# Performance work log

Measured on AMD Instinct MI355X. Metric: run time of the kernel, lower is better.

## Reference

```python
import jax, jax.numpy as jnp
import numpy as np

N_HEADS = 16
D_HEAD = 64
D_MODEL = 1024
WINDOW = 256
B, T = 4, 2048


def rotate_half(x):
    x1, x2 = jnp.split(x, 2, axis=-1)
    return jnp.concatenate([-x2, x1], axis=-1)


def apply_rope(x, cos, sin):
    return x * cos + rotate_half(x) * sin


def setup_inputs() -> dict:
    key = jax.random.key(0)
    ks = jax.random.split(key, 5)
    x = jax.random.normal(ks[0], (B, T, D_MODEL), dtype=jnp.float32)
    cos = jax.random.normal(ks[1], (1, T, 1, D_HEAD), dtype=jnp.float32)
    sin = jax.random.normal(ks[2], (1, T, 1, D_HEAD), dtype=jnp.float32)
    qkv_w = jax.random.normal(ks[3], (3 * D_MODEL, D_MODEL), dtype=jnp.float32) * (D_MODEL ** -0.5)
    out_w = jax.random.normal(ks[4], (D_MODEL, D_MODEL), dtype=jnp.float32) * (D_MODEL ** -0.5)
    return {"x": x, "cos": cos, "sin": sin, "qkv_w": qkv_w, "out_w": out_w}


def reference(x, cos, sin, qkv_w, out_w):
    Bc, Tc, C = x.shape
    # QKV projection (bias-free Linear: y = x @ W^T)
    qkv = jnp.einsum('btc,fc->btf', x, qkv_w)
    q, k, v = jnp.split(qkv, 3, axis=-1)
    # [B, H, T, d]
    def to_heads(t):
        return t.reshape(Bc, Tc, N_HEADS, D_HEAD).transpose(0, 2, 1, 3)
    q, k, v = to_heads(q), to_heads(k), to_heads(v)
    # RoPE: cos/sin [1, T, 1, d] -> [1, 1, T, d] broadcasting over heads
    cos_t = cos[:, :Tc].transpose(0, 2, 1, 3)
    sin_t = sin[:, :Tc].transpose(0, 2, 1, 3)
    q = apply_rope(q, cos_t, sin_t)
    k = apply_rope(k, cos_t, sin_t)
    # banded causal mask: allow j <= i and j >= i - (window-1)
    i = jnp.arange(Tc)[:, None]
    j = jnp.arange(Tc)[None, :]
    allowed = (j <= i) & (j >= i - (WINDOW - 1))  # [T, T]
    scale = 1.0 / jnp.sqrt(jnp.asarray(D_HEAD, dtype=q.dtype))
    scores = jnp.einsum('bhqd,bhkd->bhqk', q, k) * scale
    scores = jnp.where(allowed[None, None], scores, jnp.finfo(scores.dtype).min)
    attn = jax.nn.softmax(scores, axis=-1)
    out = jnp.einsum('bhqk,bhkd->bhqd', attn, v)
    out = out.transpose(0, 2, 1, 3).reshape(Bc, Tc, C)
    return jnp.einsum('btc,oc->bto', out, out_w)
```

## Files before the change

### kernel.cpp

```cpp
#include <hip/hip_runtime.h>

typedef __bf16 bf16_t;
typedef __bf16 bf16x8 __attribute__((ext_vector_type(8)));
typedef __bf16 bf16x4 __attribute__((ext_vector_type(4)));
typedef float f32x4 __attribute__((ext_vector_type(4)));

#define GLOAD_LDS16(gptr, lptr)                                                              \
  __builtin_amdgcn_global_load_lds((const __attribute__((address_space(1))) void*)(gptr),    \
                                   (__attribute__((address_space(3))) void*)(lptr), 16, 0, 0)

__device__ __forceinline__ f32x4 f32x4_zero() {
  f32x4 v; v[0] = 0.f; v[1] = 0.f; v[2] = 0.f; v[3] = 0.f; return v;
}

__device__ __forceinline__ int kxr(int r) { return (r & 7) ^ (((r >> 3) & 3) << 1); }

__global__ void cast3_kernel(const float* __restrict__ a, const float* __restrict__ b,
                             const float* __restrict__ c, bf16_t* __restrict__ oa,
                             bf16_t* __restrict__ ob, bf16_t* __restrict__ oc) {
  int i = blockIdx.x * blockDim.x + threadIdx.x;
  const float* src; bf16_t* dst; int j;
  if (i < 2097152) { src = a; dst = oa; j = i; }
  else if (i < 2883584) { src = b; dst = ob; j = i - 2097152; }
  else { src = c; dst = oc; j = i - 2883584; }
  float4 v = ((const float4*)src)[j];
  bf16x4 o;
  o[0] = (bf16_t)v.x; o[1] = (bf16_t)v.y; o[2] = (bf16_t)v.z; o[3] = (bf16_t)v.w;
  ((bf16x4*)dst)[j] = o;
}

template <int MODE>
__global__ __launch_bounds__(256) void gemm_bt_kernel(
    const bf16_t* __restrict__ A, const bf16_t* __restrict__ B, float* __restrict__ C,
    bf16_t* __restrict__ oq, bf16_t* __restrict__ ok_, bf16_t* __restrict__ ov,
    const float* __restrict__ cosp, const float* __restrict__ sinp,
    int M, int N, int K) {
  constexpr int BM = 128, BN = 128, BK = 32;
  __shared__ bf16_t As[BM * BK];
  __shared__ bf16_t Bs[BN * BK];
  const int tid = threadIdx.x;
  const int lane = tid & 63;
  const int wid = tid >> 6;
  const int wm = (wid >> 1) * 64;
  const int wn = (wid & 1) * 64;
  const int l16 = lane & 15;
  const int qd = lane >> 4;
  const int bm = blockIdx.x, bn = blockIdx.y;

  const int srow = tid >> 2;
  const int skol = (tid & 3) * 8;

  const bf16_t* gA = A + (size_t)(bm * BM + srow) * K + skol;
  const bf16_t* gB = B + (size_t)(bn * BN + srow) * K + skol;
  bf16_t* lA = &As[srow * BK + skol];
  bf16_t* lB = &Bs[srow * BK + skol];

  f32x4 acc[4][4];
#pragma unroll
  for (int mb = 0; mb < 4; mb++)
#pragma unroll
    for (int nb = 0; nb < 4; nb++) acc[mb][nb] = f32x4_zero();

  for (int k0 = 0; k0 < K; k0 += BK) {
    __syncthreads();
    GLOAD_LDS16(gA + k0, lA);
    GLOAD_LDS16(gA + (size_t)64 * K + k0, lA + 64 * BK);
    GLOAD_LDS16(gB + k0, lB);
    GLOAD_LDS16(gB + (size_t)64 * K + k0, lB + 64 * BK);
    __syncthreads();

    bf16x8 af[4], bfr[4];
#pragma unroll
    for (int mb = 0; mb < 4; mb++)
      af[mb] = *(const bf16x8*)&As[(wm + mb * 16 + l16) * BK + qd * 8];
#pragma unroll
    for (int nb = 0; nb < 4; nb++)
      bfr[nb] = *(const bf16x8*)&Bs[(wn + nb * 16 + l16) * BK + qd * 8];
#pragma unroll
    for (int mb = 0; mb < 4; mb++)
#pragma unroll
      for (int nb = 0; nb < 4; nb++)
        acc[mb][nb] = __builtin_amdgcn_mfma_f32_16x16x32_bf16(af[mb], bfr[nb], acc[mb][nb], 0, 0, 0);
  }

  if (MODE == 0) {
#pragma unroll
    for (int mb = 0; mb < 4; mb++)
#pragma unroll
      for (int nb = 0; nb < 4; nb++)
#pragma unroll
        for (int r = 0; r < 4; r++) {
          int row = bm * BM + wm + mb * 16 + qd * 4 + r;
          int col = bn * BN + wn + nb * 16 + l16;
          C[(size_t)row * N + col] = acc[mb][nb][r];
        }
  } else {
    const int part = bn >> 3;
    const int h = ((bn * 128 + wn) & 1023) >> 6;
    bf16_t* dst = (part == 0) ? oq : (part == 1) ? ok_ : ov;
    if (part == 2) {
#pragma unroll
      for (int mb = 0; mb < 4; mb++)
#pragma unroll
        for (int r = 0; r < 4; r++) {
          int row = bm * BM + wm + mb * 16 + qd * 4 + r;
          int b = row >> 11, t = row & 2047;
          size_t basei = (((size_t)(b * 16 + h)) * 2048 + t) * 64;
#pragma unroll
          for (int nb = 0; nb < 4; nb++)
            dst[basei + nb * 16 + l16] = (bf16_t)acc[mb][nb][r];
        }
    } else {
      const float qsc = (part == 0) ? 0.18033688011112042f : 1.0f;
#pragma unroll
      for (int mb = 0; mb < 4; mb++)
#pragma unroll
        for (int r = 0; r < 4; r++) {
          int row = bm * BM + wm + mb * 16 + qd * 4 + r;
          int b = row >> 11, t = row & 2047;
          size_t basei = (((size_t)(b * 16 + h)) * 2048 + t) * 64;
#pragma unroll
          for (int nb = 0; nb < 2; nb++) {
            int d = nb * 16 + l16;
            float xl = acc[mb][nb][r];
            float xh = acc[mb][nb + 2][r];
            float cl = cosp[t * 64 + d], ch = cosp[t * 64 + d + 32];
            float sl = sinp[t * 64 + d], sh = sinp[t * 64 + d + 32];
            dst[basei + d]      = (bf16_t)((xl * cl - xh * sl) * qsc);
            dst[basei + d + 32] = (bf16_t)((xh * ch + xl * sh) * qsc);
          }
        }
    }
  }
}

__global__ __launch_bounds__(256) void attn_kernel(
    const bf16_t* __restrict__ qh, const bf16_t* __restrict__ kh,
    const bf16_t* __restrict__ vh, bf16_t* __restrict__ ao) {
  __shared__ bf16_t qs[64 * 64];
  __shared__ bf16_t ks[64 * 64];
  __shared__ bf16_t vs[64 * 64];
  __shared__ bf16_t vswz[8 * 64 * 8];
  __shared__ bf16_t ps[4][16 * 64];

  const int tid = threadIdx.x;
  const int lane = tid & 63;
  const int wid = tid >> 6;
  const int l16 = lane & 15;
  const int qd = lane >> 4;

  const int bh = blockIdx.x;
  const int i0 = blockIdx.y * 64;
  const int b = bh >> 4, h = bh & 15;

  auto swz4 = [](int f) { int r = f >> 3; return r * 8 + ((f & 7) ^ (r & 7)); };
  const int r0 = tid >> 3, q0 = tid & 7;

  {
    const uint4* src = (const uint4*)(qh + ((size_t)bh * 2048 + i0) * 64);
    uint4* dst = (uint4*)qs;
    dst[swz4(tid)] = src[tid];
    dst[swz4(tid + 256)] = src[tid + 256];
  }

  bf16x8 bones;
#pragma unroll
  for (int e = 0; e < 8; e++) bones[e] = (bf16_t)1.0f;

  float l_i[4] = {0.f, 0.f, 0.f, 0.f};
  f32x4 oacc[4];
#pragma unroll
  for (int nb = 0; nb < 4; nb++) oacc[nb] = f32x4_zero();

  const int c1 = i0 >> 6;
  const int c0 = (c1 >= 4) ? (c1 - 4) : 0;

  for (int c = c0; c <= c1; c++) {
    const int j0 = c * 64;
    __syncthreads();
    {
      const uint4* ksrc = (const uint4*)(kh + ((size_t)bh * 2048 + j0) * 64);
      const uint4* vsrc = (const uint4*)(vh + ((size_t)bh * 2048 + j0) * 64);
      uint4* kdst = (uint4*)ks; uint4* vdst = (uint4*)vs;
      kdst[swz4(tid)] = ksrc[tid]; kdst[swz4(tid + 256)] = ksrc[tid + 256];
      vdst[r0 * 8 + (q0 ^ kxr(r0))] = vsrc[tid];
      vdst[(r0 + 32) * 8 + (q0 ^ kxr(r0 + 32))] = vsrc[tid + 256];
    }
    __syncthreads();

    f32x4 sacc[4];
#pragma unroll
    for (int nb = 0; nb < 4; nb++) sacc[nb] = f32x4_zero();
#pragma unroll
    for (int kk = 0; kk < 2; kk++) {
      bf16x8 afr = *(const bf16x8*)&qs[(wid * 16 + l16) * 64 + (((kk * 4 + qd) ^ (l16 & 7)) * 8)];
#pragma unroll
      for (int nb = 0; nb < 4; nb++) {
        bf16x8 bfr = *(const bf16x8*)&ks[(nb * 16 + l16) * 64 + (((kk * 4 + qd) ^ (l16 & 7)) * 8)];
        sacc[nb] = __builtin_amdgcn_mfma_f32_16x16x32_bf16(afr, bfr, sacc[nb], 0, 0, 0);
      }
    }

#pragma unroll
    for (int p2 = 0; p2 < 2; p2++) {
      int combo = p2 * 4 + wid;
      int jbase = (combo >> 2) * 32 + (lane >> 4) * 8;
      int dcol = (combo & 3) * 16 + (lane & 15);
      int bb = dcol >> 3, dlo = dcol & 7;
      bf16x8 v8;
#pragma unroll
      for (int e = 0; e < 8; e++) {
        int row = jbase + e;
        v8[e] = vs[row * 64 + ((bb ^ kxr(row)) * 8) + dlo];
      }
      *(bf16x8*)&vswz[(combo * 64 + lane) * 8] = v8;
    }

#pragma unroll
    for (int r = 0; r < 4; r++) {
      const int i = i0 + wid * 16 + qd * 4 + r;
      const int prow = qd * 4 + r;
#pragma unroll
      for (int nb = 0; nb < 4; nb++) {
        const int j = j0 + nb * 16 + l16;
        bool valid = (j <= i) && (j + 256 > i);
        float p = valid ? exp2f(sacc[nb][r]) : 0.f;
        ps[wid][prow * 64 + (((nb * 2 + (l16 >> 3)) ^ (prow & 7)) * 8) + (l16 & 7)] = (bf16_t)p;
      }
    }

    __syncthreads();

    f32x4 lacc = f32x4_zero();
#pragma unroll
    for (int kk = 0; kk < 2; kk++) {
      bf16x8 afr = *(const bf16x8*)&ps[wid][l16 * 64 + (((kk * 4 + qd) ^ (l16 & 7)) * 8)];
      lacc = __builtin_amdgcn_mfma_f32_16x16x32_bf16(afr, bones, lacc, 0, 0, 0);
#pragma unroll
      for (int nb = 0; nb < 4; nb++) {
        bf16x8 bfr = *(const bf16x8*)&vswz[((kk * 4 + nb) * 64 + lane) * 8];
        oacc[nb] = __builtin_amdgcn_mfma_f32_16x16x32_bf16(afr, bfr, oacc[nb], 0, 0, 0);
      }
    }
#pragma unroll
    for (int r = 0; r < 4; r++) l_i[r] += lacc[r];
  }

#pragma unroll
  for (int nb = 0; nb < 4; nb++) {
#pragma unroll
    for (int r = 0; r < 4; r++) {
      int t = i0 + wid * 16 + qd * 4 + r;
      ao[((size_t)(b * 2048 + t)) * 1024 + h * 64 + nb * 16 + l16] =
          (bf16_t)(oacc[nb][r] / l_i[r]);
    }
  }
}

extern "C" void kernel_launch(void* const* d_in, const int* in_sizes, int n_in,
                              void* d_out, int out_size, void* d_ws, size_t ws_size,
                              hipStream_t stream) {
  const float* x    = (const float*)d_in[0];
  const float* cosp = (const float*)d_in[1];
  const float* sinp = (const float*)d_in[2];
  const float* qkvw = (const float*)d_in[3];
  const float* outw = (const float*)d_in[4];
  float* out = (float*)d_out;

  char* ws = (char*)d_ws;
  bf16_t* xb  = (bf16_t*)(ws + 0);
  bf16_t* qwb = (bf16_t*)(ws + 16777216);
  bf16_t* owb = (bf16_t*)(ws + 23068672);
  bf16_t* qhp = (bf16_t*)(ws + 25165824);
  bf16_t* khp = (bf16_t*)(ws + 41943040);
  bf16_t* vhp = (bf16_t*)(ws + 58720256);
  bf16_t* aop = (bf16_t*)(ws + 75497472);

  cast3_kernel<<<12288, 256, 0, stream>>>(x, qkvw, outw, xb, qwb, owb);

  gemm_bt_kernel<1><<<dim3(64, 24), 256, 0, stream>>>(xb, qwb, nullptr, qhp, khp, vhp,
                                                      cosp, sinp, 8192, 3072, 1024);
  attn_kernel<<<dim3(64, 32), 256, 0, stream>>>(qhp, khp, vhp, aop);
  gemm_bt_kernel<0><<<dim3(64, 8), 256, 0, stream>>>(aop, owb, out, nullptr, nullptr, nullptr,
                                                     nullptr, nullptr, 8192, 1024, 1024);
}
```

Baseline: 242.9 us.

## Move RoPE from QKV GEMM epilogue into attention tile loads

Removes the RoPE and query-scaling from the QKV projection epilogue, so all Q/K/V outputs are stored uniformly without per-element cos/sin gathers. RoPE is instead applied with vectorized cos/sin loads when Q and K tiles are staged into shared memory inside the attention kernel. This simplifies the GEMM epilogue but recomputes RoPE on each K chunk for every query block that reuses it, and applies rotation to bf16-rounded values rather than fp32 accumulators.

```diff
diff --git a/kernel.cpp b/kernel.cpp
--- a/kernel.cpp
+++ b/kernel.cpp
@@ -14,6 +14,30 @@
 }
 
 __device__ __forceinline__ int kxr(int r) { return (r & 7) ^ (((r >> 3) & 3) << 1); }
+
+__device__ __forceinline__ void rope8(const bf16x8 xl, const bf16x8 xh,
+                                      const float* __restrict__ cosb,
+                                      const float* __restrict__ sinb, float sc,
+                                      bf16x8& ol, bf16x8& oh) {
+  float4 cl0 = *(const float4*)(cosb);
+  float4 cl1 = *(const float4*)(cosb + 4);
+  float4 ch0 = *(const float4*)(cosb + 32);
+  float4 ch1 = *(const float4*)(cosb + 36);
+  float4 sl0 = *(const float4*)(sinb);
+  float4 sl1 = *(const float4*)(sinb + 4);
+  float4 sh0 = *(const float4*)(sinb + 32);
+  float4 sh1 = *(const float4*)(sinb + 36);
+  float cl[8] = {cl0.x, cl0.y, cl0.z, cl0.w, cl1.x, cl1.y, cl1.z, cl1.w};
+  float ch[8] = {ch0.x, ch0.y, ch0.z, ch0.w, ch1.x, ch1.y, ch1.z, ch1.w};
+  float sl[8] = {sl0.x, sl0.y, sl0.z, sl0.w, sl1.x, sl1.y, sl1.z, sl1.w};
+  float sh[8] = {sh0.x, sh0.y, sh0.z, sh0.w, sh1.x, sh1.y, sh1.z, sh1.w};
+#pragma unroll
+  for (int e = 0; e < 8; e++) {
+    float a = (float)xl[e], b = (float)xh[e];
+    ol[e] = (bf16_t)((a * cl[e] - b * sl[e]) * sc);
+    oh[e] = (bf16_t)((b * ch[e] + a * sh[e]) * sc);
+  }
+}
 
 __global__ void cast3_kernel(const float* __restrict__ a, const float* __restrict__ b,
                              const float* __restrict__ c, bf16_t* __restrict__ oa,
@@ -33,7 +57,6 @@
 __global__ __launch_bounds__(256) void gemm_bt_kernel(
     const bf16_t* __restrict__ A, const bf16_t* __restrict__ B, float* __restrict__ C,
     bf16_t* __restrict__ oq, bf16_t* __restrict__ ok_, bf16_t* __restrict__ ov,
-    const float* __restrict__ cosp, const float* __restrict__ sinp,
     int M, int N, int K) {
   constexpr int BM = 128, BN = 128, BK = 32;
   __shared__ bf16_t As[BM * BK];
@@ -98,45 +121,24 @@
     const int part = bn >> 3;
     const int h = ((bn * 128 + wn) & 1023) >> 6;
     bf16_t* dst = (part == 0) ? oq : (part == 1) ? ok_ : ov;
-    if (part == 2) {
-#pragma unroll
-      for (int mb = 0; mb < 4; mb++)
-#pragma unroll
-        for (int r = 0; r < 4; r++) {
-          int row = bm * BM + wm + mb * 16 + qd * 4 + r;
-          int b = row >> 11, t = row & 2047;
-          size_t basei = (((size_t)(b * 16 + h)) * 2048 + t) * 64;
-#pragma unroll
-          for (int nb = 0; nb < 4; nb++)
-            dst[basei + nb * 16 + l16] = (bf16_t)acc[mb][nb][r];
-        }
-    } else {
-      const float qsc = (part == 0) ? 0.18033688011112042f : 1.0f;
-#pragma unroll
-      for (int mb = 0; mb < 4; mb++)
-#pragma unroll
-        for (int r = 0; r < 4; r++) {
-          int row = bm * BM + wm + mb * 16 + qd * 4 + r;
-          int b = row >> 11, t = row & 2047;
-          size_t basei = (((size_t)(b * 16 + h)) * 2048 + t) * 64;
-#pragma unroll
-          for (int nb = 0; nb < 2; nb++) {
-            int d = nb * 16 + l16;
-            float xl = acc[mb][nb][r];
-            float xh = acc[mb][nb + 2][r];
-            float cl = cosp[t * 64 + d], ch = cosp[t * 64 + d + 32];
-            float sl = sinp[t * 64 + d], sh = sinp[t * 64 + d + 32];
-            dst[basei + d]      = (bf16_t)((xl * cl - xh * sl) * qsc);
-            dst[basei + d + 32] = (bf16_t)((xh * ch + xl * sh) * qsc);
-          }
-        }
-    }
+#pragma unroll
+    for (int mb = 0; mb < 4; mb++)
+#pragma unroll
+      for (int r = 0; r < 4; r++) {
+        int row = bm * BM + wm + mb * 16 + qd * 4 + r;
+        int b = row >> 11, t = row & 2047;
+        size_t basei = (((size_t)(b * 16 + h)) * 2048 + t) * 64;
+#pragma unroll
+        for (int nb = 0; nb < 4; nb++)
+          dst[basei + nb * 16 + l16] = (bf16_t)acc[mb][nb][r];
+      }
   }
 }
 
 __global__ __launch_bounds__(256) void attn_kernel(
     const bf16_t* __restrict__ qh, const bf16_t* __restrict__ kh,
-    const bf16_t* __restrict__ vh, bf16_t* __restrict__ ao) {
+    const bf16_t* __restrict__ vh, bf16_t* __restrict__ ao,
+    const float* __restrict__ cosp, const float* __restrict__ sinp) {
   __shared__ bf16_t qs[64 * 64];
   __shared__ bf16_t ks[64 * 64];
   __shared__ bf16_t vs[64 * 64];
@@ -155,12 +157,17 @@
 
   auto swz4 = [](int f) { int r = f >> 3; return r * 8 + ((f & 7) ^ (r & 7)); };
   const int r0 = tid >> 3, q0 = tid & 7;
+  const int rr = tid >> 2, qo = tid & 3;
 
   {
-    const uint4* src = (const uint4*)(qh + ((size_t)bh * 2048 + i0) * 64);
-    uint4* dst = (uint4*)qs;
-    dst[swz4(tid)] = src[tid];
-    dst[swz4(tid + 256)] = src[tid + 256];
+    const bf16x8* src = (const bf16x8*)(qh + ((size_t)bh * 2048 + i0) * 64);
+    bf16x8* dst = (bf16x8*)qs;
+    const int fl = rr * 8 + qo, fh = fl + 4;
+    bf16x8 ol, oh;
+    rope8(src[fl], src[fh], cosp + (i0 + rr) * 64 + qo * 8, sinp + (i0 + rr) * 64 + qo * 8,
+          0.18033688011112042f, ol, oh);
+    dst[swz4(fl)] = ol;
+    dst[swz4(fh)] = oh;
   }
 
   bf16x8 bones;
@@ -179,10 +186,16 @@
     const int j0 = c * 64;
     __syncthreads();
     {
-      const uint4* ksrc = (const uint4*)(kh + ((size_t)bh * 2048 + j0) * 64);
+      const bf16x8* ksrc = (const bf16x8*)(kh + ((size_t)bh * 2048 + j0) * 64);
       const uint4* vsrc = (const uint4*)(vh + ((size_t)bh * 2048 + j0) * 64);
-      uint4* kdst = (uint4*)ks; uint4* vdst = (uint4*)vs;
-      kdst[swz4(tid)] = ksrc[tid]; kdst[swz4(tid + 256)] = ksrc[tid + 256];
+      bf16x8* kdst = (bf16x8*)ks;
+      uint4* vdst = (uint4*)vs;
+      const int fl = rr * 8 + qo, fh = fl + 4;
+      bf16x8 ol, oh;
+      rope8(ksrc[fl], ksrc[fh], cosp + (j0 + rr) * 64 + qo * 8, sinp + (j0 + rr) * 64 + qo * 8,
+            1.0f, ol, oh);
+      kdst[swz4(fl)] = ol;
+      kdst[swz4(fh)] = oh;
       vdst[r0 * 8 + (q0 ^ kxr(r0))] = vsrc[tid];
       vdst[(r0 + 32) * 8 + (q0 ^ kxr(r0 + 32))] = vsrc[tid + 256];
     }
@@ -279,8 +292,8 @@
   cast3_kernel<<<12288, 256, 0, stream>>>(x, qkvw, outw, xb, qwb, owb);
 
   gemm_bt_kernel<1><<<dim3(64, 24), 256, 0, stream>>>(xb, qwb, nullptr, qhp, khp, vhp,
-                                                      cosp, sinp, 8192, 3072, 1024);
-  attn_kernel<<<dim3(64, 32), 256, 0, stream>>>(qhp, khp, vhp, aop);
+                                                      8192, 3072, 1024);
+  attn_kernel<<<dim3(64, 32), 256, 0, stream>>>(qhp, khp, vhp, aop, cosp, sinp);
   gemm_bt_kernel<0><<<dim3(64, 8), 256, 0, stream>>>(aop, owb, out, nullptr, nullptr, nullptr,
-                                                     nullptr, nullptr, 8192, 1024, 1024);
-}
+                                                     8192, 1024, 1024);
+}
```

Measured after the change: 244.7 us. Within noise of the previous version (+0.7%).
